# Optimization experiments

Hardware: AMD Instinct MI355X
Metric: run time of the kernel (lower is better)

Reference implementation:

```python
import jax, jax.numpy as jnp
import numpy as np

B, S, E, H, D = 4, 1024, 192, 64, 3  # head_dim pinned to 3 by the rotation matmul


def setup_inputs() -> dict:
    key = jax.random.key(0)
    k = jax.random.split(key, 6)
    x = jax.random.normal(k[0], (B, S, E), dtype=jnp.float32)
    w_scale = 1.0 / np.sqrt(E).astype(np.float32)
    Wq = jax.random.uniform(k[1], (E, E), jnp.float32, -w_scale, w_scale)
    Wk = jax.random.uniform(k[2], (E, E), jnp.float32, -w_scale, w_scale)
    Wv = jax.random.uniform(k[3], (E, E), jnp.float32, -w_scale, w_scale)
    Wo = jax.random.uniform(k[4], (E, E), jnp.float32, -w_scale, w_scale)
    rot = jax.random.normal(k[5], (H, D, D), dtype=jnp.float32)  # (num_heads, head_dim, 3), head_dim==3
    return {"x": x, "Wq": Wq, "Wk": Wk, "Wv": Wv, "Wo": Wo, "rot": rot}


def reference(x, Wq, Wk, Wv, Wo, rot):
    b, s, e = x.shape
    h, d, _ = rot.shape
    # projections (torch Linear: y = x @ W.T), split heads -> (b, h, s, d)
    q = jnp.einsum('bse,oe->bso', x, Wq).reshape(b, s, h, d).swapaxes(1, 2)
    k = jnp.einsum('bse,oe->bso', x, Wk).reshape(b, s, h, d).swapaxes(1, 2)
    v = jnp.einsum('bse,oe->bso', x, Wv).reshape(b, s, h, d).swapaxes(1, 2)
    # per-head learnable rotation folded into q and k
    q = jnp.einsum('bhsd,hde->bhse', q, rot)
    k = jnp.einsum('bhsd,hde->bhse', k, rot)
    scores = jnp.einsum('bhqd,bhkd->bhqk', q, k) / jnp.sqrt(jnp.asarray(d, x.dtype))
    attn = jax.nn.softmax(scores, axis=-1)
    out = jnp.einsum('bhqk,bhkd->bhqd', attn, v)  # (b, h, s, d)
    out = out.swapaxes(1, 2).reshape(b, s, e)
    return jnp.einsum('bse,oe->bso', out, Wo)
```

## Files before the change

### kernel.cpp

```cpp
#include <hip/hip_runtime.h>
#include <hip/hip_bf16.h>

#define BB 4
#define SS 1024
#define EE 192
#define HH 64

constexpr int BH = BB * HH;

typedef __attribute__((ext_vector_type(8))) short bs8;
typedef __attribute__((ext_vector_type(16))) float fx16;
union U4B { uint4 u; bs8 s; };

constexpr size_t OFF_QF  = 0;
constexpr size_t OFF_KF  = OFF_QF  + (size_t)BH*SS*2;
constexpr size_t OFF_VC  = OFF_KF  + (size_t)BH*SS*2;
constexpr size_t OFF_AO  = OFF_VC  + (size_t)BH*SS*3/2;
constexpr size_t OFF_WCH = OFF_AO  + (size_t)BB*SS*EE;
constexpr size_t OFF_WCL = OFF_WCH + (size_t)576*EE/2;
constexpr size_t OFF_WOH = OFF_WCL + (size_t)576*EE/2;
constexpr size_t OFF_WOL = OFF_WOH + (size_t)EE*EE/2;

static __device__ __forceinline__ float fast_exp2(float x) {
#if __has_builtin(__builtin_amdgcn_exp2f)
  return __builtin_amdgcn_exp2f(x);
#else
  return exp2f(x);
#endif
}
static __device__ __forceinline__ float fast_rcp(float x) {
#if __has_builtin(__builtin_amdgcn_rcpf)
  return __builtin_amdgcn_rcpf(x);
#else
  return 1.0f / x;
#endif
}

static __device__ __forceinline__ void split2(float a, float b, unsigned& hi, unsigned& lo) {
  unsigned h;
  asm("v_cvt_pk_bf16_f32 %0, %1, %2" : "=v"(h) : "v"(a), "v"(b));
  float ha = __uint_as_float(h << 16);
  float hb = __uint_as_float(h & 0xFFFF0000u);
  float la = a - ha, lb = b - hb;
  unsigned l;
  asm("v_cvt_pk_bf16_f32 %0, %1, %2" : "=v"(l) : "v"(la), "v"(lb));
  hi = h; lo = l;
}

__global__ __launch_bounds__(256) void fold_split_k(
    const float* __restrict__ Wq, const float* __restrict__ Wk,
    const float* __restrict__ Wv, const float* __restrict__ Wo,
    const float* __restrict__ rot,
    __hip_bfloat16* __restrict__ Wch, __hip_bfloat16* __restrict__ Wcl,
    __hip_bfloat16* __restrict__ Woh, __hip_bfloat16* __restrict__ Wol)
{
  int t = blockIdx.x * 256 + threadIdx.x;
  float val;
  __hip_bfloat16 *ph, *pl;
  int idx;
  if (t < 576 * EE) {
    int o = t / EE, e = t - o * EE;
    int s3 = o / 192, oo = o - s3 * 192;
    int h = oo / 3, ep = oo - h * 3;
    if (s3 == 2) {
      val = Wv[(size_t)oo * EE + e];
    } else {
      const float* W = s3 ? Wk : Wq;
      float acc = 0.f;
#pragma unroll
      for (int d = 0; d < 3; ++d)
        acc += rot[h * 9 + d * 3 + ep] * W[(size_t)(h * 3 + d) * EE + e];
      val = acc * (s3 ? 1.0f : 0.8329876360019913f);
    }
    ph = Wch; pl = Wcl; idx = t;
  } else {
    int u = t - 576 * EE;
    if (u >= EE * EE) return;
    val = Wo[u]; ph = Woh; pl = Wol; idx = u;
  }
  __hip_bfloat16 hi = __float2bfloat16(val);
  float lo = val - __bfloat162float(hi);
  ph[idx] = hi;
  pl[idx] = __float2bfloat16(lo);
}

__global__ __launch_bounds__(256) void gemm_qkv_k(
    const float* __restrict__ x,
    const unsigned short* __restrict__ Wch, const unsigned short* __restrict__ Wcl,
    __hip_bfloat16* __restrict__ Qf, __hip_bfloat16* __restrict__ Kf,
    __hip_bfloat16* __restrict__ Vc)
{
  __shared__ __align__(16) short xsh[64][72], xsl[64][72];
  __shared__ __align__(16) short wsh[64][72], wsl[64][72];
  int colBase = blockIdx.x * 64;
  int rowBase = blockIdx.y * 64;
  int t = threadIdx.x;
  int lane = t & 63, w = t >> 6;
  int wr = w >> 1, wc = w & 1;
  int l31 = lane & 31, lh = lane >> 5;

  const fx16 zc = {0,0,0,0, 0,0,0,0, 0,0,0,0, 0,0,0,0};
  fx16 acc = zc;

  int srow = t >> 2, sk = (t & 3) * 16;

  for (int kk = 0; kk < 3; ++kk) {
    const float4* xg = (const float4*)&x[(size_t)(rowBase + srow) * EE + kk * 64 + sk];
    float4 v0 = xg[0], v1 = xg[1], v2 = xg[2], v3 = xg[3];
    const uint4* whg = (const uint4*)&Wch[(size_t)(colBase + srow) * EE + kk * 64 + sk];
    const uint4* wlg = (const uint4*)&Wcl[(size_t)(colBase + srow) * EE + kk * 64 + sk];
    uint4 wh0 = whg[0], wh1 = whg[1], wl0 = wlg[0], wl1 = wlg[1];

    unsigned hu[8], lu[8];
    split2(v0.x, v0.y, hu[0], lu[0]); split2(v0.z, v0.w, hu[1], lu[1]);
    split2(v1.x, v1.y, hu[2], lu[2]); split2(v1.z, v1.w, hu[3], lu[3]);
    split2(v2.x, v2.y, hu[4], lu[4]); split2(v2.z, v2.w, hu[5], lu[5]);
    split2(v3.x, v3.y, hu[6], lu[6]); split2(v3.z, v3.w, hu[7], lu[7]);

    __syncthreads();
    *(uint4*)&xsh[srow][sk]     = make_uint4(hu[0], hu[1], hu[2], hu[3]);
    *(uint4*)&xsh[srow][sk + 8] = make_uint4(hu[4], hu[5], hu[6], hu[7]);
    *(uint4*)&xsl[srow][sk]     = make_uint4(lu[0], lu[1], lu[2], lu[3]);
    *(uint4*)&xsl[srow][sk + 8] = make_uint4(lu[4], lu[5], lu[6], lu[7]);
    *(uint4*)&wsh[srow][sk]     = wh0;
    *(uint4*)&wsh[srow][sk + 8] = wh1;
    *(uint4*)&wsl[srow][sk]     = wl0;
    *(uint4*)&wsl[srow][sk + 8] = wl1;
    __syncthreads();

#pragma unroll
    for (int ks = 0; ks < 4; ++ks) {
      int ac = ks * 16 + lh * 8;
      U4B Ah, Al, Bh, Bl;
      Ah.u = *(const uint4*)&xsh[wr * 32 + l31][ac];
      Al.u = *(const uint4*)&xsl[wr * 32 + l31][ac];
      Bh.u = *(const uint4*)&wsh[wc * 32 + l31][ac];
      Bl.u = *(const uint4*)&wsl[wc * 32 + l31][ac];
      acc = __builtin_amdgcn_mfma_f32_32x32x16_bf16(Ah.s, Bh.s, acc, 0, 0, 0);
      acc = __builtin_amdgcn_mfma_f32_32x32x16_bf16(Al.s, Bh.s, acc, 0, 0, 0);
      acc = __builtin_amdgcn_mfma_f32_32x32x16_bf16(Ah.s, Bl.s, acc, 0, 0, 0);
    }
  }

  int o = colBase + wc * 32 + l31;
  int s3 = o / 192, oo = o - s3 * 192;
  int hh = oo / 3, d = oo - hh * 3;
#pragma unroll
  for (int r = 0; r < 16; ++r) {
    int row = rowBase + wr * 32 + (r & 3) + 8 * (r >> 2) + 4 * lh;
    int b = row >> 10, s = row & (SS - 1);
    size_t bh = (size_t)(b * HH + hh);
    float v = acc[r];
    if (s3 == 0) {
      Qf[(bh * SS + s) * 4 + d] = __float2bfloat16(v);
      if (d == 2) Qf[(bh * SS + s) * 4 + 3] = __float2bfloat16(0.0f);
    } else if (s3 == 1) {
      Kf[(bh * SS + s) * 4 + d] = __float2bfloat16(v);
      if (d == 2) Kf[(bh * SS + s) * 4 + 3] = __float2bfloat16(0.0f);
    } else {
      Vc[bh * (3 * SS) + (size_t)d * SS + s] = __float2bfloat16(v);
    }
  }
}

__global__ __launch_bounds__(256, 4) void attn_k(
    const unsigned short* __restrict__ Qfg, const unsigned short* __restrict__ Kfg,
    const unsigned short* __restrict__ Vcg, float* __restrict__ AO)
{
  __shared__ __align__(16) short KfL[1024 * 4];
  __shared__ __align__(16) short VcL[4 * 1040];
  int bh = blockIdx.x & 255;
  int eighth = blockIdx.x >> 8;
  int b = bh >> 6, h = bh & 63;

  const uint2* ksrc = (const uint2*)Kfg + (size_t)bh * 1024;
  uint2* kdst = (uint2*)KfL;
  for (int i = threadIdx.x; i < 1024; i += 256) kdst[i] = ksrc[i];
  const uint4* vsrc = (const uint4*)Vcg + (size_t)bh * 384;
  for (int i = threadIdx.x; i < 384; i += 256) {
    int r = i >> 7, cq = i & 127;
    *(uint4*)(VcL + r * 1040 + cq * 8) = vsrc[i];
  }
  {
    unsigned v1 = 0x3F803F80u;
    for (int i = threadIdx.x; i < 128; i += 256)
      *(uint4*)(VcL + 3 * 1040 + i * 8) = make_uint4(v1, v1, v1, v1);
  }
  __syncthreads();

  int lane = threadIdx.x & 63, w = threadIdx.x >> 6;
  int h32 = lane >> 5;
  int col = lane & 31;
  int q32 = eighth * 128 + w * 32;

  uint2 qq = *(const uint2*)(Qfg + ((size_t)bh * SS + q32 + col) * 4);
  U4B bq; bq.u = make_uint4(h32 ? 0u : qq.x, h32 ? 0u : qq.y, 0u, 0u);

  const fx16 zc = {0,0,0,0, 0,0,0,0, 0,0,0,0, 0,0,0,0};
  fx16 accPV = zc;
  int vbase = (col & 3) * 1040 + 8 * h32;

#pragma unroll 2
  for (int kt = 0; kt < 32; ++kt) {
    uint2 kk = *(const uint2*)(KfL + (size_t)(kt * 32 + col) * 4);
    U4B ak; ak.u = make_uint4(kk.x, kk.y, 0u, 0u);
    U4B bv1; bv1.u = *(const uint4*)(VcL + vbase + kt * 32);
    U4B bv2; bv2.u = *(const uint4*)(VcL + vbase + kt * 32 + 16);

    fx16 S = __builtin_amdgcn_mfma_f32_32x32x16_bf16(ak.s, bq.s, zc, 0, 0, 0);
#pragma unroll
    for (int i = 0; i < 16; ++i) S[i] = fast_exp2(S[i]);
    unsigned u0, u1, u2, u3, u4, u5, u6, u7;
    asm("v_cvt_pk_bf16_f32 %0, %1, %2" : "=v"(u0) : "v"(S[0]),  "v"(S[1]));
    asm("v_cvt_pk_bf16_f32 %0, %1, %2" : "=v"(u1) : "v"(S[2]),  "v"(S[3]));
    asm("v_cvt_pk_bf16_f32 %0, %1, %2" : "=v"(u2) : "v"(S[4]),  "v"(S[5]));
    asm("v_cvt_pk_bf16_f32 %0, %1, %2" : "=v"(u3) : "v"(S[6]),  "v"(S[7]));
    asm("v_cvt_pk_bf16_f32 %0, %1, %2" : "=v"(u4) : "v"(S[8]),  "v"(S[9]));
    asm("v_cvt_pk_bf16_f32 %0, %1, %2" : "=v"(u5) : "v"(S[10]), "v"(S[11]));
    asm("v_cvt_pk_bf16_f32 %0, %1, %2" : "=v"(u6) : "v"(S[12]), "v"(S[13]));
    asm("v_cvt_pk_bf16_f32 %0, %1, %2" : "=v"(u7) : "v"(S[14]), "v"(S[15]));
    asm("v_permlane32_swap_b32 %0, %1" : "+v"(u0), "+v"(u2));
    asm("v_permlane32_swap_b32 %0, %1" : "+v"(u1), "+v"(u3));
    asm("v_permlane32_swap_b32 %0, %1" : "+v"(u4), "+v"(u6));
    asm("v_permlane32_swap_b32 %0, %1" : "+v"(u5), "+v"(u7));
    U4B p1; p1.u = make_uint4(u0, u1, u2, u3);
    U4B p2; p2.u = make_uint4(u4, u5, u6, u7);
    accPV = __builtin_amdgcn_mfma_f32_32x32x16_bf16(p1.s, bv1.s, accPV, 0, 0, 0);
    accPV = __builtin_amdgcn_mfma_f32_32x32x16_bf16(p2.s, bv2.s, accPV, 0, 0, 0);
  }

  int base3 = (lane & 32) | 3;
  float inv[16];
#pragma unroll
  for (int rg = 0; rg < 16; ++rg)
    inv[rg] = __shfl(fast_rcp(accPV[rg]), base3, 64);
  if (col < 3) {
#pragma unroll
    for (int rg = 0; rg < 16; ++rg) {
      int row = (rg & 3) + 8 * (rg >> 2) + 4 * h32;
      AO[((size_t)(b * SS + q32 + row)) * EE + h * 3 + col] = accPV[rg] * inv[rg];
    }
  }
}

__global__ __launch_bounds__(256) void gemm_out_k(
    const float* __restrict__ AO,
    const unsigned short* __restrict__ Woh, const unsigned short* __restrict__ Wol,
    float* __restrict__ out)
{
  __shared__ __align__(16) short xsh[64][72], xsl[64][72];
  __shared__ __align__(16) short wsh[64][72], wsl[64][72];
  int colBase = blockIdx.x * 64;
  int rowBase = blockIdx.y * 64;
  int t = threadIdx.x;
  int lane = t & 63, w = t >> 6;
  int wr = w >> 1, wc = w & 1;
  int l31 = lane & 31, lh = lane >> 5;

  const fx16 zc = {0,0,0,0, 0,0,0,0, 0,0,0,0, 0,0,0,0};
  fx16 acc = zc;

  int srow = t >> 2, sk = (t & 3) * 16;

  for (int kk = 0; kk < 3; ++kk) {
    const float4* xg = (const float4*)&AO[(size_t)(rowBase + srow) * EE + kk * 64 + sk];
    float4 v0 = xg[0], v1 = xg[1], v2 = xg[2], v3 = xg[3];
    const uint4* whg = (const uint4*)&Woh[(size_t)(colBase + srow) * EE + kk * 64 + sk];
    const uint4* wlg = (const uint4*)&Wol[(size_t)(colBase + srow) * EE + kk * 64 + sk];
    uint4 wh0 = whg[0], wh1 = whg[1], wl0 = wlg[0], wl1 = wlg[1];

    unsigned hu[8], lu[8];
    split2(v0.x, v0.y, hu[0], lu[0]); split2(v0.z, v0.w, hu[1], lu[1]);
    split2(v1.x, v1.y, hu[2], lu[2]); split2(v1.z, v1.w, hu[3], lu[3]);
    split2(v2.x, v2.y, hu[4], lu[4]); split2(v2.z, v2.w, hu[5], lu[5]);
    split2(v3.x, v3.y, hu[6], lu[6]); split2(v3.z, v3.w, hu[7], lu[7]);

    __syncthreads();
    *(uint4*)&xsh[srow][sk]     = make_uint4(hu[0], hu[1], hu[2], hu[3]);
    *(uint4*)&xsh[srow][sk + 8] = make_uint4(hu[4], hu[5], hu[6], hu[7]);
    *(uint4*)&xsl[srow][sk]     = make_uint4(lu[0], lu[1], lu[2], lu[3]);
    *(uint4*)&xsl[srow][sk + 8] = make_uint4(lu[4], lu[5], lu[6], lu[7]);
    *(uint4*)&wsh[srow][sk]     = wh0;
    *(uint4*)&wsh[srow][sk + 8] = wh1;
    *(uint4*)&wsl[srow][sk]     = wl0;
    *(uint4*)&wsl[srow][sk + 8] = wl1;
    __syncthreads();

#pragma unroll
    for (int ks = 0; ks < 4; ++ks) {
      int ac = ks * 16 + lh * 8;
      U4B Ah, Al, Bh, Bl;
      Ah.u = *(const uint4*)&xsh[wr * 32 + l31][ac];
      Al.u = *(const uint4*)&xsl[wr * 32 + l31][ac];
      Bh.u = *(const uint4*)&wsh[wc * 32 + l31][ac];
      Bl.u = *(const uint4*)&wsl[wc * 32 + l31][ac];
      acc = __builtin_amdgcn_mfma_f32_32x32x16_bf16(Ah.s, Bh.s, acc, 0, 0, 0);
      acc = __builtin_amdgcn_mfma_f32_32x32x16_bf16(Al.s, Bh.s, acc, 0, 0, 0);
      acc = __builtin_amdgcn_mfma_f32_32x32x16_bf16(Ah.s, Bl.s, acc, 0, 0, 0);
    }
  }

  int o = colBase + wc * 32 + l31;
#pragma unroll
  for (int r = 0; r < 16; ++r) {
    int row = rowBase + wr * 32 + (r & 3) + 8 * (r >> 2) + 4 * lh;
    out[(size_t)row * EE + o] = acc[r];
  }
}

extern "C" void kernel_launch(void* const* d_in, const int* in_sizes, int n_in,
                              void* d_out, int out_size, void* d_ws, size_t ws_size,
                              hipStream_t stream) {
  const float* x   = (const float*)d_in[0];
  const float* Wq  = (const float*)d_in[1];
  const float* Wk  = (const float*)d_in[2];
  const float* Wv  = (const float*)d_in[3];
  const float* Wo  = (const float*)d_in[4];
  const float* rot = (const float*)d_in[5];
  float* ws  = (float*)d_ws;
  unsigned short* Qf  = (unsigned short*)(ws + OFF_QF);
  unsigned short* Kf  = (unsigned short*)(ws + OFF_KF);
  unsigned short* Vc  = (unsigned short*)(ws + OFF_VC);
  float* AO  = ws + OFF_AO;
  unsigned short* Wch = (unsigned short*)(ws + OFF_WCH);
  unsigned short* Wcl = (unsigned short*)(ws + OFF_WCL);
  unsigned short* Woh = (unsigned short*)(ws + OFF_WOH);
  unsigned short* Wol = (unsigned short*)(ws + OFF_WOL);
  float* out = (float*)d_out;

  fold_split_k<<<dim3((576 * EE + EE * EE) / 256), 256, 0, stream>>>(
      Wq, Wk, Wv, Wo, rot,
      (__hip_bfloat16*)Wch, (__hip_bfloat16*)Wcl,
      (__hip_bfloat16*)Woh, (__hip_bfloat16*)Wol);
  gemm_qkv_k<<<dim3(9, 64), 256, 0, stream>>>(x, Wch, Wcl,
                                              (__hip_bfloat16*)Qf, (__hip_bfloat16*)Kf,
                                              (__hip_bfloat16*)Vc);
  attn_k<<<dim3(BH * 8), 256, 0, stream>>>(Qf, Kf, Vc, AO);
  gemm_out_k<<<dim3(3, 64), 256, 0, stream>>>(AO, Woh, Wol, out);
}
```

Baseline: 64.35 us.

## Fuse weight rotation folding and bf16 splitting into the GEMM kernels

Removes the separate fold_split_k launch and instead has each GEMM block read the fp32 weights directly, apply the per-head rotation and Q scale, and split into bf16 hi/lo pairs in registers before staging to shared memory. This drops one kernel launch and the workspace round-trip for the folded weights. In exchange every row-tile block redoes the fold and split of the weight tile, adding three fp32 loads per element for Q/K. The unroll-2 pragma on the attention inner loop is also removed.

```diff
diff --git a/kernel.cpp b/kernel.cpp
--- a/kernel.cpp
+++ b/kernel.cpp
@@ -16,10 +16,6 @@
 constexpr size_t OFF_KF  = OFF_QF  + (size_t)BH*SS*2;
 constexpr size_t OFF_VC  = OFF_KF  + (size_t)BH*SS*2;
 constexpr size_t OFF_AO  = OFF_VC  + (size_t)BH*SS*3/2;
-constexpr size_t OFF_WCH = OFF_AO  + (size_t)BB*SS*EE;
-constexpr size_t OFF_WCL = OFF_WCH + (size_t)576*EE/2;
-constexpr size_t OFF_WOH = OFF_WCL + (size_t)576*EE/2;
-constexpr size_t OFF_WOL = OFF_WOH + (size_t)EE*EE/2;
 
 static __device__ __forceinline__ float fast_exp2(float x) {
 #if __has_builtin(__builtin_amdgcn_exp2f)
@@ -47,69 +43,76 @@
   hi = h; lo = l;
 }
 
-__global__ __launch_bounds__(256) void fold_split_k(
-    const float* __restrict__ Wq, const float* __restrict__ Wk,
-    const float* __restrict__ Wv, const float* __restrict__ Wo,
-    const float* __restrict__ rot,
-    __hip_bfloat16* __restrict__ Wch, __hip_bfloat16* __restrict__ Wcl,
-    __hip_bfloat16* __restrict__ Woh, __hip_bfloat16* __restrict__ Wol)
-{
-  int t = blockIdx.x * 256 + threadIdx.x;
-  float val;
-  __hip_bfloat16 *ph, *pl;
-  int idx;
-  if (t < 576 * EE) {
-    int o = t / EE, e = t - o * EE;
-    int s3 = o / 192, oo = o - s3 * 192;
-    int h = oo / 3, ep = oo - h * 3;
-    if (s3 == 2) {
-      val = Wv[(size_t)oo * EE + e];
-    } else {
-      const float* W = s3 ? Wk : Wq;
-      float acc = 0.f;
-#pragma unroll
-      for (int d = 0; d < 3; ++d)
-        acc += rot[h * 9 + d * 3 + ep] * W[(size_t)(h * 3 + d) * EE + e];
-      val = acc * (s3 ? 1.0f : 0.8329876360019913f);
-    }
-    ph = Wch; pl = Wcl; idx = t;
-  } else {
-    int u = t - 576 * EE;
-    if (u >= EE * EE) return;
-    val = Wo[u]; ph = Woh; pl = Wol; idx = u;
-  }
-  __hip_bfloat16 hi = __float2bfloat16(val);
-  float lo = val - __bfloat162float(hi);
-  ph[idx] = hi;
-  pl[idx] = __float2bfloat16(lo);
-}
-
 __global__ __launch_bounds__(256) void gemm_qkv_k(
     const float* __restrict__ x,
-    const unsigned short* __restrict__ Wch, const unsigned short* __restrict__ Wcl,
+    const float* __restrict__ Wq, const float* __restrict__ Wk,
+    const float* __restrict__ Wv, const float* __restrict__ rot,
     __hip_bfloat16* __restrict__ Qf, __hip_bfloat16* __restrict__ Kf,
     __hip_bfloat16* __restrict__ Vc)
 {
   __shared__ __align__(16) short xsh[64][72], xsl[64][72];
   __shared__ __align__(16) short wsh[64][72], wsl[64][72];
-  int colBase = blockIdx.x * 64;
+  int bx = blockIdx.x;
+  int colBase = bx * 64;
   int rowBase = blockIdx.y * 64;
   int t = threadIdx.x;
   int lane = t & 63, w = t >> 6;
   int wr = w >> 1, wc = w & 1;
   int l31 = lane & 31, lh = lane >> 5;
+  int s3 = bx / 3;
 
   const fx16 zc = {0,0,0,0, 0,0,0,0, 0,0,0,0, 0,0,0,0};
   fx16 acc = zc;
 
   int srow = t >> 2, sk = (t & 3) * 16;
 
+  int o = colBase + srow;
+  int oo = o - s3 * 192;
+  int hh2 = oo / 3, ep = oo - hh2 * 3;
+  const float *w0p, *w1p = nullptr, *w2p = nullptr;
+  float rr0 = 0.f, rr1 = 0.f, rr2 = 0.f, wscale = 1.0f;
+  if (s3 < 2) {
+    const float* W = s3 ? Wk : Wq;
+    wscale = s3 ? 1.0f : 0.8329876360019913f;
+    rr0 = rot[hh2 * 9 + 0 + ep];
+    rr1 = rot[hh2 * 9 + 3 + ep];
+    rr2 = rot[hh2 * 9 + 6 + ep];
+    w0p = W + (size_t)(hh2 * 3 + 0) * EE;
+    w1p = W + (size_t)(hh2 * 3 + 1) * EE;
+    w2p = W + (size_t)(hh2 * 3 + 2) * EE;
+  } else {
+    w0p = Wv + (size_t)oo * EE;
+  }
+
   for (int kk = 0; kk < 3; ++kk) {
-    const float4* xg = (const float4*)&x[(size_t)(rowBase + srow) * EE + kk * 64 + sk];
+    int off = kk * 64 + sk;
+    const float4* xg = (const float4*)&x[(size_t)(rowBase + srow) * EE + off];
     float4 v0 = xg[0], v1 = xg[1], v2 = xg[2], v3 = xg[3];
-    const uint4* whg = (const uint4*)&Wch[(size_t)(colBase + srow) * EE + kk * 64 + sk];
-    const uint4* wlg = (const uint4*)&Wcl[(size_t)(colBase + srow) * EE + kk * 64 + sk];
-    uint4 wh0 = whg[0], wh1 = whg[1], wl0 = wlg[0], wl1 = wlg[1];
+
+    unsigned whu[8], wlu[8];
+    if (s3 < 2) {
+      const float4* a4 = (const float4*)(w0p + off);
+      const float4* b4 = (const float4*)(w1p + off);
+      const float4* c4 = (const float4*)(w2p + off);
+#pragma unroll
+      for (int i = 0; i < 4; ++i) {
+        float4 a = a4[i], bb = b4[i], c = c4[i];
+        float f0 = fmaf(rr2, c.x, fmaf(rr1, bb.x, rr0 * a.x)) * wscale;
+        float f1 = fmaf(rr2, c.y, fmaf(rr1, bb.y, rr0 * a.y)) * wscale;
+        float f2 = fmaf(rr2, c.z, fmaf(rr1, bb.z, rr0 * a.z)) * wscale;
+        float f3 = fmaf(rr2, c.w, fmaf(rr1, bb.w, rr0 * a.w)) * wscale;
+        split2(f0, f1, whu[2 * i], wlu[2 * i]);
+        split2(f2, f3, whu[2 * i + 1], wlu[2 * i + 1]);
+      }
+    } else {
+      const float4* a4 = (const float4*)(w0p + off);
+#pragma unroll
+      for (int i = 0; i < 4; ++i) {
+        float4 a = a4[i];
+        split2(a.x, a.y, whu[2 * i], wlu[2 * i]);
+        split2(a.z, a.w, whu[2 * i + 1], wlu[2 * i + 1]);
+      }
+    }
 
     unsigned hu[8], lu[8];
     split2(v0.x, v0.y, hu[0], lu[0]); split2(v0.z, v0.w, hu[1], lu[1]);
@@ -122,10 +125,10 @@
     *(uint4*)&xsh[srow][sk + 8] = make_uint4(hu[4], hu[5], hu[6], hu[7]);
     *(uint4*)&xsl[srow][sk]     = make_uint4(lu[0], lu[1], lu[2], lu[3]);
     *(uint4*)&xsl[srow][sk + 8] = make_uint4(lu[4], lu[5], lu[6], lu[7]);
-    *(uint4*)&wsh[srow][sk]     = wh0;
-    *(uint4*)&wsh[srow][sk + 8] = wh1;
-    *(uint4*)&wsl[srow][sk]     = wl0;
-    *(uint4*)&wsl[srow][sk + 8] = wl1;
+    *(uint4*)&wsh[srow][sk]     = make_uint4(whu[0], whu[1], whu[2], whu[3]);
+    *(uint4*)&wsh[srow][sk + 8] = make_uint4(whu[4], whu[5], whu[6], whu[7]);
+    *(uint4*)&wsl[srow][sk]     = make_uint4(wlu[0], wlu[1], wlu[2], wlu[3]);
+    *(uint4*)&wsl[srow][sk + 8] = make_uint4(wlu[4], wlu[5], wlu[6], wlu[7]);
     __syncthreads();
 
 #pragma unroll
@@ -142,19 +145,19 @@
     }
   }
 
-  int o = colBase + wc * 32 + l31;
-  int s3 = o / 192, oo = o - s3 * 192;
-  int hh = oo / 3, d = oo - hh * 3;
+  int oc = colBase + wc * 32 + l31;
+  int os3 = oc / 192, ooc = oc - os3 * 192;
+  int hhc = ooc / 3, d = ooc - hhc * 3;
 #pragma unroll
   for (int r = 0; r < 16; ++r) {
     int row = rowBase + wr * 32 + (r & 3) + 8 * (r >> 2) + 4 * lh;
     int b = row >> 10, s = row & (SS - 1);
-    size_t bh = (size_t)(b * HH + hh);
+    size_t bh = (size_t)(b * HH + hhc);
     float v = acc[r];
-    if (s3 == 0) {
+    if (os3 == 0) {
       Qf[(bh * SS + s) * 4 + d] = __float2bfloat16(v);
       if (d == 2) Qf[(bh * SS + s) * 4 + 3] = __float2bfloat16(0.0f);
-    } else if (s3 == 1) {
+    } else if (os3 == 1) {
       Kf[(bh * SS + s) * 4 + d] = __float2bfloat16(v);
       if (d == 2) Kf[(bh * SS + s) * 4 + 3] = __float2bfloat16(0.0f);
     } else {
@@ -200,7 +203,6 @@
   fx16 accPV = zc;
   int vbase = (col & 3) * 1040 + 8 * h32;
 
-#pragma unroll 2
   for (int kt = 0; kt < 32; ++kt) {
     uint2 kk = *(const uint2*)(KfL + (size_t)(kt * 32 + col) * 4);
     U4B ak; ak.u = make_uint4(kk.x, kk.y, 0u, 0u);
@@ -244,8 +246,7 @@
 }
 
 __global__ __launch_bounds__(256) void gemm_out_k(
-    const float* __restrict__ AO,
-    const unsigned short* __restrict__ Woh, const unsigned short* __restrict__ Wol,
+    const float* __restrict__ AO, const float* __restrict__ Wo,
     float* __restrict__ out)
 {
   __shared__ __align__(16) short xsh[64][72], xsl[64][72];
@@ -261,29 +262,34 @@
   fx16 acc = zc;
 
   int srow = t >> 2, sk = (t & 3) * 16;
+  const float* wrow = Wo + (size_t)(colBase + srow) * EE;
 
   for (int kk = 0; kk < 3; ++kk) {
-    const float4* xg = (const float4*)&AO[(size_t)(rowBase + srow) * EE + kk * 64 + sk];
+    int off = kk * 64 + sk;
+    const float4* xg = (const float4*)&AO[(size_t)(rowBase + srow) * EE + off];
     float4 v0 = xg[0], v1 = xg[1], v2 = xg[2], v3 = xg[3];
-    const uint4* whg = (const uint4*)&Woh[(size_t)(colBase + srow) * EE + kk * 64 + sk];
-    const uint4* wlg = (const uint4*)&Wol[(size_t)(colBase + srow) * EE + kk * 64 + sk];
-    uint4 wh0 = whg[0], wh1 = whg[1], wl0 = wlg[0], wl1 = wlg[1];
-
-    unsigned hu[8], lu[8];
+    const float4* wg = (const float4*)(wrow + off);
+    float4 w0 = wg[0], w1 = wg[1], w2 = wg[2], w3 = wg[3];
+
+    unsigned hu[8], lu[8], whu[8], wlu[8];
     split2(v0.x, v0.y, hu[0], lu[0]); split2(v0.z, v0.w, hu[1], lu[1]);
     split2(v1.x, v1.y, hu[2], lu[2]); split2(v1.z, v1.w, hu[3], lu[3]);
     split2(v2.x, v2.y, hu[4], lu[4]); split2(v2.z, v2.w, hu[5], lu[5]);
     split2(v3.x, v3.y, hu[6], lu[6]); split2(v3.z, v3.w, hu[7], lu[7]);
+    split2(w0.x, w0.y, whu[0], wlu[0]); split2(w0.z, w0.w, whu[1], wlu[1]);
+    split2(w1.x, w1.y, whu[2], wlu[2]); split2(w1.z, w1.w, whu[3], wlu[3]);
+    split2(w2.x, w2.y, whu[4], wlu[4]); split2(w2.z, w2.w, whu[5], wlu[5]);
+    split2(w3.x, w3.y, whu[6], wlu[6]); split2(w3.z, w3.w, whu[7], wlu[7]);
 
     __syncthreads();
     *(uint4*)&xsh[srow][sk]     = make_uint4(hu[0], hu[1], hu[2], hu[3]);
     *(uint4*)&xsh[srow][sk + 8] = make_uint4(hu[4], hu[5], hu[6], hu[7]);
     *(uint4*)&xsl[srow][sk]     = make_uint4(lu[0], lu[1], lu[2], lu[3]);
     *(uint4*)&xsl[srow][sk + 8] = make_uint4(lu[4], lu[5], lu[6], lu[7]);
-    *(uint4*)&wsh[srow][sk]     = wh0;
-    *(uint4*)&wsh[srow][sk + 8] = wh1;
-    *(uint4*)&wsl[srow][sk]     = wl0;
-    *(uint4*)&wsl[srow][sk + 8] = wl1;
+    *(uint4*)&wsh[srow][sk]     = make_uint4(whu[0], whu[1], whu[2], whu[3]);
+    *(uint4*)&wsh[srow][sk + 8] = make_uint4(whu[4], whu[5], whu[6], whu[7]);
+    *(uint4*)&wsl[srow][sk]     = make_uint4(wlu[0], wlu[1], wlu[2], wlu[3]);
+    *(uint4*)&wsl[srow][sk + 8] = make_uint4(wlu[4], wlu[5], wlu[6], wlu[7]);
     __syncthreads();
 
 #pragma unroll
@@ -322,19 +328,11 @@
   unsigned short* Kf  = (unsigned short*)(ws + OFF_KF);
   unsigned short* Vc  = (unsigned short*)(ws + OFF_VC);
   float* AO  = ws + OFF_AO;
-  unsigned short* Wch = (unsigned short*)(ws + OFF_WCH);
-  unsigned short* Wcl = (unsigned short*)(ws + OFF_WCL);
-  unsigned short* Woh = (unsigned short*)(ws + OFF_WOH);
-  unsigned short* Wol = (unsigned short*)(ws + OFF_WOL);
   float* out = (float*)d_out;
 
-  fold_split_k<<<dim3((576 * EE + EE * EE) / 256), 256, 0, stream>>>(
-      Wq, Wk, Wv, Wo, rot,
-      (__hip_bfloat16*)Wch, (__hip_bfloat16*)Wcl,
-      (__hip_bfloat16*)Woh, (__hip_bfloat16*)Wol);
-  gemm_qkv_k<<<dim3(9, 64), 256, 0, stream>>>(x, Wch, Wcl,
+  gemm_qkv_k<<<dim3(9, 64), 256, 0, stream>>>(x, Wq, Wk, Wv, rot,
                                               (__hip_bfloat16*)Qf, (__hip_bfloat16*)Kf,
                                               (__hip_bfloat16*)Vc);
   attn_k<<<dim3(BH * 8), 256, 0, stream>>>(Qf, Kf, Vc, AO);
-  gemm_out_k<<<dim3(3, 64), 256, 0, stream>>>(AO, Woh, Wol, out);
-}
+  gemm_out_k<<<dim3(3, 64), 256, 0, stream>>>(AO, Wo, out);
+}
```

Result: no change. 63.75 us (-0.9%).
